# Optimization experiments

Measured on AMD Instinct MI355X. Metric: run time of the kernel, lower is better.

Reference implementation:

```python
import jax, jax.numpy as jnp
import numpy as np

N = 50000
E = 1600000
IN_CH = 128
HID = 16
HEADS = 8
OUT_CH = 1
NEG_SLOPE = 0.2


def setup_inputs() -> dict:
    key = jax.random.key(0)
    ks = jax.random.split(key, 12)
    x = jax.random.normal(ks[0], (N, IN_CH), dtype=jnp.float32)
    edge_index = jax.random.randint(ks[1], (2, E), 0, N, dtype=jnp.int64)
    s1 = 1.0 / np.sqrt(IN_CH)
    s2 = 1.0 / np.sqrt(HEADS * HID)
    W1 = jax.random.normal(ks[2], (IN_CH, HEADS * HID), dtype=jnp.float32) * s1
    att_src1 = jax.random.normal(ks[3], (HEADS, HID), dtype=jnp.float32) * s1
    att_dst1 = jax.random.normal(ks[4], (HEADS, HID), dtype=jnp.float32) * s1
    b1 = jnp.zeros((HEADS * HID,), dtype=jnp.float32)
    W2 = jax.random.normal(ks[5], (HEADS * HID, OUT_CH), dtype=jnp.float32) * s2
    att_src2 = jax.random.normal(ks[6], (1, OUT_CH), dtype=jnp.float32) * s2
    att_dst2 = jax.random.normal(ks[7], (1, OUT_CH), dtype=jnp.float32) * s2
    b2 = jnp.zeros((OUT_CH,), dtype=jnp.float32)
    return {"x": x, "edge_index": edge_index,
            "W1": W1, "att_src1": att_src1, "att_dst1": att_dst1, "b1": b1,
            "W2": W2, "att_src2": att_src2, "att_dst2": att_dst2, "b2": b2}


def gat_conv(x, src, dst, W, att_src, att_dst, b, heads, concat):
    n = x.shape[0]
    h = (x @ W).reshape(n, heads, -1)               # [N, H, C]
    a_s = jnp.einsum('nhc,hc->nh', h, att_src)      # [N, H]
    a_d = jnp.einsum('nhc,hc->nh', h, att_dst)
    e = jax.nn.leaky_relu(a_s[src] + a_d[dst], NEG_SLOPE)  # [E, H]
    # segment softmax over incoming edges of each dst node
    emax = jax.ops.segment_max(e, dst, num_segments=n)
    p = jnp.exp(e - emax[dst])
    denom = jax.ops.segment_sum(p, dst, num_segments=n)
    alpha = p / (denom[dst] + 1e-16)                 # [E, H]
    msg = h[src] * alpha[:, :, None]                 # [E, H, C]
    out = jax.ops.segment_sum(msg, dst, num_segments=n)  # [N, H, C]
    if concat:
        out = out.reshape(n, -1)
    else:
        out = out.mean(axis=1)
    return out + b


def reference(x, edge_index, W1, att_src1, att_dst1, b1, W2, att_src2, att_dst2, b2):
    n = x.shape[0]
    loops = jnp.arange(n, dtype=edge_index.dtype)
    src = jnp.concatenate([edge_index[0], loops])    # PyG add_self_loops=True
    dst = jnp.concatenate([edge_index[1], loops])
    h = gat_conv(x, src, dst, W1, att_src1, att_dst1, b1, HEADS, True)
    h = jax.nn.elu(h)
    out = gat_conv(h, src, dst, W2, att_src2, att_dst2, b2, 1, False)
    return out
```

## Files before the change

### kernel.cpp

```cpp
#include <hip/hip_runtime.h>
#include <hip/hip_fp16.h>
#include <math.h>

#define N_NODES 50000
#define N_EDGES 1600000
#define NEG 0.2f

#define PB 256
#define CHUNK ((N_EDGES + PB - 1) / PB)
#define BSHIFT 6
#define NBUCK ((N_NODES + 63) >> BSHIFT)


__global__ __launch_bounds__(1024) void count_pass(const int* __restrict__ ei, int* __restrict__ counts) {
    __shared__ int h[NBUCK];
    for (int i = threadIdx.x; i < NBUCK; i += 1024) h[i] = 0;
    __syncthreads();
    int p = blockIdx.x;
    int e0 = p * CHUNK, e1 = min(e0 + CHUNK, N_EDGES);
    for (int e = e0 + threadIdx.x; e < e1; e += 1024) {
        int d = ei[N_EDGES + e];
        atomicAdd(&h[d >> BSHIFT], 1);
    }
    __syncthreads();
    for (int i = threadIdx.x; i < NBUCK; i += 1024) counts[p * NBUCK + i] = h[i];
}

__global__ __launch_bounds__(256) void scan_blocks(const int* __restrict__ counts,
                                                   int* __restrict__ starts, int* __restrict__ btot) {
    __shared__ int s[256];
    int b = blockIdx.x;
    int v = counts[threadIdx.x * NBUCK + b];
    s[threadIdx.x] = v;
    __syncthreads();
    for (int off = 1; off < 256; off <<= 1) {
        int t = (threadIdx.x >= off) ? s[threadIdx.x - off] : 0;
        __syncthreads();
        s[threadIdx.x] += t;
        __syncthreads();
    }
    starts[threadIdx.x * NBUCK + b] = s[threadIdx.x] - v;
    if (threadIdx.x == 255) btot[b] = s[255];
}

__global__ __launch_bounds__(1024) void scan_total(const int* __restrict__ btot, int* __restrict__ bbase) {
    __shared__ int s[1024];
    int t = threadIdx.x;
    int v = (t < NBUCK) ? btot[t] : 0;
    s[t] = v;
    __syncthreads();
    for (int off = 1; off < 1024; off <<= 1) {
        int x = (t >= off) ? s[t - off] : 0;
        __syncthreads();
        s[t] += x;
        __syncthreads();
    }
    if (t < NBUCK) bbase[t] = s[t] - v;
    if (t == 0) bbase[NBUCK] = N_EDGES;
}

__global__ __launch_bounds__(1024) void bin_scatter(const int* __restrict__ ei, const int* __restrict__ starts,
                                                    const int* __restrict__ bbase, int* __restrict__ temp) {
    __shared__ int cur[NBUCK];
    int p = blockIdx.x;
    for (int i = threadIdx.x; i < NBUCK; i += 1024)
        cur[i] = bbase[i] + starts[p * NBUCK + i];
    __syncthreads();
    int e0 = p * CHUNK, e1 = min(e0 + CHUNK, N_EDGES);
    for (int e = e0 + threadIdx.x; e < e1; e += 1024) {
        int s = ei[e];
        int d = ei[N_EDGES + e];
        int b = d >> BSHIFT;
        int pos = atomicAdd(&cur[b], 1);
        temp[pos] = s | ((d & 63) << 16);
    }
}

__global__ __launch_bounds__(256) void csr_build(const int* __restrict__ temp, const int* __restrict__ bbase,
                                                 int* __restrict__ rowptr, int* __restrict__ csr_src) {
    __shared__ int cnt[64];
    __shared__ int cur[64];
    int b = blockIdx.x;
    int base = bbase[b];
    int nE = bbase[b + 1] - base;
    if (threadIdx.x < 64) cnt[threadIdx.x] = 0;
    __syncthreads();
    for (int i = threadIdx.x; i < nE; i += 256)
        atomicAdd(&cnt[temp[base + i] >> 16], 1);
    __syncthreads();
    if (threadIdx.x < 64) {
        int v = cnt[threadIdx.x];
        int incl = v;
#pragma unroll
        for (int off = 1; off < 64; off <<= 1) {
            int u = __shfl_up(incl, off, 64);
            if (threadIdx.x >= off) incl += u;
        }
        int excl = incl - v;
        cur[threadIdx.x] = base + excl;
        int node = (b << BSHIFT) + threadIdx.x;
        if (node <= N_NODES) rowptr[node] = base + excl;
    }
    __syncthreads();
    for (int i = threadIdx.x; i < nE; i += 256) {
        int v = temp[base + i];
        int pos = atomicAdd(&cur[v >> 16], 1);
        csr_src[pos] = v & 0xFFFF;
    }
}


__global__ __launch_bounds__(256) void gemm1_kernel(const float* __restrict__ x, const float* __restrict__ W1,
                                                    const float* __restrict__ att_s, const float* __restrict__ att_d,
                                                    __half2* __restrict__ h1, float* __restrict__ as1,
                                                    float* __restrict__ ad1) {
    __shared__ float xs[128][36];
    int n0 = blockIdx.x * 32;
    int t = threadIdx.x;
#pragma unroll
    for (int i = 0; i < 16; ++i) {
        int f = i * 256 + t;
        int r = f >> 7, c = f & 127;
        int gr = n0 + r;
        float v = (gr < N_NODES) ? x[(size_t)gr * 128 + c] : 0.f;
        xs[c][r] = v;
    }
    __syncthreads();
    int c0 = (t & 31) * 4;
    int r0 = (t >> 5) * 4;
    float acc[4][4];
#pragma unroll
    for (int i = 0; i < 4; ++i)
#pragma unroll
        for (int j = 0; j < 4; ++j) acc[i][j] = 0.f;
#pragma unroll 4
    for (int k = 0; k < 128; ++k) {
        float4 w = *(const float4*)(W1 + k * 128 + c0);
        float4 xr = *(const float4*)(&xs[k][r0]);
        float xv[4] = {xr.x, xr.y, xr.z, xr.w};
        float wv[4] = {w.x, w.y, w.z, w.w};
#pragma unroll
        for (int i = 0; i < 4; ++i)
#pragma unroll
            for (int j = 0; j < 4; ++j) acc[i][j] += xv[i] * wv[j];
    }
#pragma unroll
    for (int i = 0; i < 4; ++i) {
        int row = n0 + r0 + i;
        if (row < N_NODES) {
            __half2 p0 = __float22half2_rn(make_float2(acc[i][0], acc[i][1]));
            __half2 p1 = __float22half2_rn(make_float2(acc[i][2], acc[i][3]));
            h1[(size_t)row * 64 + (c0 >> 1)] = p0;
            h1[(size_t)row * 64 + (c0 >> 1) + 1] = p1;
        }
    }
    int head = (t & 31) >> 2;
    float ps[4], pd[4];
#pragma unroll
    for (int i = 0; i < 4; ++i) {
        float s = 0.f, d = 0.f;
#pragma unroll
        for (int j = 0; j < 4; ++j) {
            s += acc[i][j] * att_s[c0 + j];
            d += acc[i][j] * att_d[c0 + j];
        }
        ps[i] = s; pd[i] = d;
    }
#pragma unroll
    for (int i = 0; i < 4; ++i) {
        ps[i] += __shfl_xor(ps[i], 1, 64);
        ps[i] += __shfl_xor(ps[i], 2, 64);
        pd[i] += __shfl_xor(pd[i], 1, 64);
        pd[i] += __shfl_xor(pd[i], 2, 64);
    }
    if ((t & 3) == 0) {
#pragma unroll
        for (int i = 0; i < 4; ++i) {
            int row = n0 + r0 + i;
            if (row < N_NODES) {
                as1[row * 8 + head] = ps[i];
                ad1[row * 8 + head] = pd[i];
            }
        }
    }
}


__device__ __forceinline__ float lrelu(float v) { return fmaxf(v, NEG * v); }

__global__ __launch_bounds__(256) void agg1_kernel(const char* __restrict__ h1c, const char* __restrict__ as1c,
                                                   const float* __restrict__ ad1, const int* __restrict__ rowptr,
                                                   const int* __restrict__ csr_src, const float* __restrict__ b1,
                                                   const float* __restrict__ W2, float* __restrict__ h2out) {
    int lane = threadIdx.x & 63;
    int n = blockIdx.x * 4 + (threadIdx.x >> 6);
    if (n >= N_NODES) return;
    int hB = lane >> 3;
    int hP = lane & 7;
    unsigned lane4 = (unsigned)lane << 2;
    unsigned hP4 = (unsigned)hP << 2;
    int bperm_base = hB << 2;

    float adP = ad1[n * 8 + hP];
    float adC = ad1[n * 8 + hB];
    float asC = *(const float*)(as1c + ((unsigned)n * 32u + ((unsigned)hB << 2)));
    float p_self = __expf(lrelu(asC + adC));
    __half2 hvs = *(const __half2*)(h1c + (((unsigned)n << 8) + lane4));
    float acc0 = p_self * __half2float(__low2half(hvs));
    float acc1 = p_self * __half2float(__high2half(hvs));
    float l = p_self;

    int jb = rowptr[n], je = rowptr[n + 1];
    int deg = je - jb;
    int nchunks = deg >> 3;
    int j = jb;
    if (nchunks > 0) {
        int sP = csr_src[j + (lane >> 3)];
        float aP = *(const float*)(as1c + (((unsigned)sP << 5) + hP4));
        for (int c = 0; c < nchunks; ++c) {
            float pP = __expf(lrelu(aP + adP));
            int pPi = __float_as_int(pP);
            int sPc = sP;
            if (c + 1 < nchunks) {
                sP = csr_src[j + 8 + (lane >> 3)];
                aP = *(const float*)(as1c + (((unsigned)sP << 5) + hP4));
            }
#pragma unroll
            for (int e = 0; e < 8; ++e) {
                int addr = bperm_base + e * 32;
                float p = __int_as_float(__builtin_amdgcn_ds_bpermute(addr, pPi));
                int s = __builtin_amdgcn_ds_bpermute(addr, sPc);
                __half2 hv = *(const __half2*)(h1c + (((unsigned)s << 8) + lane4));
                acc0 += p * __half2float(__low2half(hv));
                acc1 += p * __half2float(__high2half(hv));
                l += p;
            }
            j += 8;
        }
    }
    if (j < je) {
        int r = je - j;
        int myj = j + (lane >> 3);
        int sP = 0;
        float pP = 0.f;
        if (myj < je) {
            sP = csr_src[myj];
            float aP = *(const float*)(as1c + (((unsigned)sP << 5) + hP4));
            pP = __expf(lrelu(aP + adP));
        }
        int pPi = __float_as_int(pP);
        for (int e = 0; e < r; ++e) {
            int addr = bperm_base + e * 32;
            float p = __int_as_float(__builtin_amdgcn_ds_bpermute(addr, pPi));
            int s = __builtin_amdgcn_ds_bpermute(addr, sP);
            __half2 hv = *(const __half2*)(h1c + (((unsigned)s << 8) + lane4));
            acc0 += p * __half2float(__low2half(hv));
            acc1 += p * __half2float(__high2half(hv));
            l += p;
        }
    }

    float inv = 1.f / (l + 1e-16f);
    int c0 = lane * 2;
    float y0 = acc0 * inv + b1[c0];
    float y1 = acc1 * inv + b1[c0 + 1];
    y0 = y0 > 0.f ? y0 : expm1f(y0);
    y1 = y1 > 0.f ? y1 : expm1f(y1);
    float part = y0 * W2[c0] + y1 * W2[c0 + 1];
    for (int off = 32; off; off >>= 1) part += __shfl_down(part, off, 64);
    if (lane == 0) h2out[n] = part;
}


__global__ __launch_bounds__(256) void agg2_kernel(const float* __restrict__ h2, const int* __restrict__ rowptr,
                                                   const int* __restrict__ csr_src, const float* __restrict__ att_s2,
                                                   const float* __restrict__ att_d2, const float* __restrict__ b2,
                                                   float* __restrict__ out) {
    int sub = threadIdx.x & 31;
    int n = blockIdx.x * 8 + (threadIdx.x >> 5);
    if (n >= N_NODES) return;
    float asw = att_s2[0], adw = att_d2[0];
    float h2n = h2[n];
    float ad = h2n * adw;
    float acc = 0.f, l = 0.f;
    if (sub == 0) {
        float p = __expf(lrelu(h2n * asw + ad));
        acc = p * h2n;
        l = p;
    }
    int jb = rowptr[n], je = rowptr[n + 1];
    for (int j = jb + sub; j < je; j += 32) {
        int s = csr_src[j];
        float hs = h2[s];
        float p = __expf(lrelu(hs * asw + ad));
        acc += p * hs;
        l += p;
    }
#pragma unroll
    for (int off = 16; off; off >>= 1) {
        acc += __shfl_down(acc, off, 32);
        l += __shfl_down(l, off, 32);
    }
    if (sub == 0) out[n] = acc / (l + 1e-16f) + b2[0];
}


extern "C" void kernel_launch(void* const* d_in, const int* in_sizes, int n_in,
                              void* d_out, int out_size, void* d_ws, size_t ws_size,
                              hipStream_t stream) {
    const float* x = (const float*)d_in[0];
    const int* ei = (const int*)d_in[1];
    const float* W1 = (const float*)d_in[2];
    const float* att_s1 = (const float*)d_in[3];
    const float* att_d1 = (const float*)d_in[4];
    const float* b1 = (const float*)d_in[5];
    const float* W2 = (const float*)d_in[6];
    const float* att_s2 = (const float*)d_in[7];
    const float* att_d2 = (const float*)d_in[8];
    const float* b2 = (const float*)d_in[9];
    float* out = (float*)d_out;

    char* p = (char*)d_ws;
    auto alloc = [&](size_t bytes) {
        char* q = p;
        p += (bytes + 255) & ~(size_t)255;
        return q;
    };
    int* counts = (int*)alloc((size_t)PB * NBUCK * 4);
    int* starts = (int*)alloc((size_t)PB * NBUCK * 4);
    int* btot = (int*)alloc((size_t)NBUCK * 4);
    int* bbase = (int*)alloc((size_t)(NBUCK + 1) * 4);
    int* rowptr = (int*)alloc((size_t)(N_NODES + 1) * 4);
    int* csr_src = (int*)alloc((size_t)N_EDGES * 4);
    __half2* h1 = (__half2*)alloc((size_t)N_NODES * 128 * 2);
    int* temp = (int*)h1;
    float* as1 = (float*)alloc((size_t)N_NODES * 8 * 4);
    float* ad1 = (float*)alloc((size_t)N_NODES * 8 * 4);
    float* h2 = (float*)alloc((size_t)N_NODES * 4);

    count_pass<<<PB, 1024, 0, stream>>>(ei, counts);
    scan_blocks<<<NBUCK, 256, 0, stream>>>(counts, starts, btot);
    scan_total<<<1, 1024, 0, stream>>>(btot, bbase);
    bin_scatter<<<PB, 1024, 0, stream>>>(ei, starts, bbase, temp);
    csr_build<<<NBUCK, 256, 0, stream>>>(temp, bbase, rowptr, csr_src);
    gemm1_kernel<<<(N_NODES + 31) / 32, 256, 0, stream>>>(x, W1, att_s1, att_d1, h1, as1, ad1);
    agg1_kernel<<<(N_NODES + 3) / 4, 256, 0, stream>>>((const char*)h1, (const char*)as1, ad1, rowptr,
                                                       csr_src, b1, W2, h2);
    agg2_kernel<<<(N_NODES + 7) / 8, 256, 0, stream>>>(h2, rowptr, csr_src, att_s2, att_d2, b2, out);
}
```

Measured before the change: 232.7 us.

## Locally sort edge chunks in LDS before coalesced bucket scatter

The binning scatter kernel now sorts each chunk of edges by destination bucket in shared memory, using a local histogram and scan. Each wave then writes whole bucket runs to global memory contiguously, replacing the scattered per-edge global stores. The partition count is halved to 128 so each chunk of 12500 ints (about 50KB) fits in LDS alongside the counters. The cost is fewer, heavier blocks with 256 threads and high LDS use, which limits occupancy, plus a duplicated count pass inside the scatter kernel.

```diff
diff --git a/kernel.cpp b/kernel.cpp
--- a/kernel.cpp
+++ b/kernel.cpp
@@ -6,8 +6,8 @@
 #define N_EDGES 1600000
 #define NEG 0.2f
 
-#define PB 256
-#define CHUNK ((N_EDGES + PB - 1) / PB)
+#define PB 128
+#define CHUNK (N_EDGES / PB)
 #define BSHIFT 6
 #define NBUCK ((N_NODES + 63) >> BSHIFT)
 
@@ -17,8 +17,8 @@
     for (int i = threadIdx.x; i < NBUCK; i += 1024) h[i] = 0;
     __syncthreads();
     int p = blockIdx.x;
-    int e0 = p * CHUNK, e1 = min(e0 + CHUNK, N_EDGES);
-    for (int e = e0 + threadIdx.x; e < e1; e += 1024) {
+    int e0 = p * CHUNK;
+    for (int e = e0 + threadIdx.x; e < e0 + CHUNK; e += 1024) {
         int d = ei[N_EDGES + e];
         atomicAdd(&h[d >> BSHIFT], 1);
     }
@@ -30,17 +30,18 @@
                                                    int* __restrict__ starts, int* __restrict__ btot) {
     __shared__ int s[256];
     int b = blockIdx.x;
-    int v = counts[threadIdx.x * NBUCK + b];
-    s[threadIdx.x] = v;
+    int t = threadIdx.x;
+    int v = (t < PB) ? counts[t * NBUCK + b] : 0;
+    s[t] = v;
     __syncthreads();
     for (int off = 1; off < 256; off <<= 1) {
-        int t = (threadIdx.x >= off) ? s[threadIdx.x - off] : 0;
-        __syncthreads();
-        s[threadIdx.x] += t;
-        __syncthreads();
-    }
-    starts[threadIdx.x * NBUCK + b] = s[threadIdx.x] - v;
-    if (threadIdx.x == 255) btot[b] = s[255];
+        int u = (t >= off) ? s[t - off] : 0;
+        __syncthreads();
+        s[t] += u;
+        __syncthreads();
+    }
+    if (t < PB) starts[t * NBUCK + b] = s[t] - v;
+    if (t == 255) btot[b] = s[255];
 }
 
 __global__ __launch_bounds__(1024) void scan_total(const int* __restrict__ btot, int* __restrict__ bbase) {
@@ -59,20 +60,62 @@
     if (t == 0) bbase[NBUCK] = N_EDGES;
 }
 
-__global__ __launch_bounds__(1024) void bin_scatter(const int* __restrict__ ei, const int* __restrict__ starts,
+__global__ __launch_bounds__(256) void sort_scatter(const int* __restrict__ ei, const int* __restrict__ starts,
                                                     const int* __restrict__ bbase, int* __restrict__ temp) {
+    __shared__ int cnt[NBUCK];
+    __shared__ int loff[NBUCK];
     __shared__ int cur[NBUCK];
-    int p = blockIdx.x;
-    for (int i = threadIdx.x; i < NBUCK; i += 1024)
-        cur[i] = bbase[i] + starts[p * NBUCK + i];
-    __syncthreads();
-    int e0 = p * CHUNK, e1 = min(e0 + CHUNK, N_EDGES);
-    for (int e = e0 + threadIdx.x; e < e1; e += 1024) {
+    __shared__ int sbuf[256];
+    __shared__ int ldata[CHUNK];
+    int p = blockIdx.x, t = threadIdx.x;
+    for (int i = t; i < NBUCK; i += 256) cnt[i] = 0;
+    __syncthreads();
+    int e0 = p * CHUNK;
+    for (int e = e0 + t; e < e0 + CHUNK; e += 256) {
+        int d = ei[N_EDGES + e];
+        atomicAdd(&cnt[d >> BSHIFT], 1);
+    }
+    __syncthreads();
+    int base = t * 4;
+    int c[4];
+    int sum = 0;
+#pragma unroll
+    for (int k = 0; k < 4; ++k) {
+        int b = base + k;
+        c[k] = (b < NBUCK) ? cnt[b] : 0;
+        sum += c[k];
+    }
+    sbuf[t] = sum;
+    __syncthreads();
+    for (int off = 1; off < 256; off <<= 1) {
+        int u = (t >= off) ? sbuf[t - off] : 0;
+        __syncthreads();
+        sbuf[t] += u;
+        __syncthreads();
+    }
+    int run = sbuf[t] - sum;
+#pragma unroll
+    for (int k = 0; k < 4; ++k) {
+        int b = base + k;
+        if (b < NBUCK) {
+            loff[b] = run;
+            cur[b] = run;
+            run += c[k];
+        }
+    }
+    __syncthreads();
+    for (int e = e0 + t; e < e0 + CHUNK; e += 256) {
         int s = ei[e];
         int d = ei[N_EDGES + e];
-        int b = d >> BSHIFT;
-        int pos = atomicAdd(&cur[b], 1);
-        temp[pos] = s | ((d & 63) << 16);
+        int pos = atomicAdd(&cur[d >> BSHIFT], 1);
+        ldata[pos] = s | ((d & 63) << 16);
+    }
+    __syncthreads();
+    int wv = t >> 6, ln = t & 63;
+    for (int b = wv; b < NBUCK; b += 4) {
+        int l0 = loff[b], len = cnt[b];
+        int g0 = bbase[b] + starts[p * NBUCK + b];
+        for (int k = ln; k < len; k += 64) temp[g0 + k] = ldata[l0 + k];
     }
 }
 
@@ -341,7 +384,7 @@
     count_pass<<<PB, 1024, 0, stream>>>(ei, counts);
     scan_blocks<<<NBUCK, 256, 0, stream>>>(counts, starts, btot);
     scan_total<<<1, 1024, 0, stream>>>(btot, bbase);
-    bin_scatter<<<PB, 1024, 0, stream>>>(ei, starts, bbase, temp);
+    sort_scatter<<<PB, 256, 0, stream>>>(ei, starts, bbase, temp);
     csr_build<<<NBUCK, 256, 0, stream>>>(temp, bbase, rowptr, csr_src);
     gemm1_kernel<<<(N_NODES + 31) / 32, 256, 0, stream>>>(x, W1, att_s1, att_d1, h1, as1, ad1);
     agg1_kernel<<<(N_NODES + 3) / 4, 256, 0, stream>>>((const char*)h1, (const char*)as1, ad1, rowptr,
```

Result: slower. 288.9 us (+24.1%).

## Fuse per-bucket CSR build into aggregation kernels using LDS-local edge lists

Applied to the files above, without the earlier changes.

Removes the separate csr_build kernel and its global rowptr/csr_src arrays. Each aggregation block now takes one 64-node bucket of binned edges, counts and sorts them into shared memory, and then aggregates those nodes from the LDS edge list. This saves a kernel launch and a global write and re-read of the CSR arrays, but the bucket sort is redone in both agg1 and agg2. The fixed LDSE=2816 buffer assumes no bucket holds more edges than that, which holds for uniform random graphs but could overflow otherwise. Parallelism drops to 782 blocks, each wave handling 8 nodes in sequence, and the old prefetch of the next chunk's sources is gone.

```diff
diff --git a/kernel.cpp b/kernel.cpp
--- a/kernel.cpp
+++ b/kernel.cpp
@@ -10,6 +10,7 @@
 #define CHUNK ((N_EDGES + PB - 1) / PB)
 #define BSHIFT 6
 #define NBUCK ((N_NODES + 63) >> BSHIFT)
+#define LDSE 2816
 
 
 __global__ __launch_bounds__(1024) void count_pass(const int* __restrict__ ei, int* __restrict__ counts) {
@@ -30,17 +31,18 @@
                                                    int* __restrict__ starts, int* __restrict__ btot) {
     __shared__ int s[256];
     int b = blockIdx.x;
-    int v = counts[threadIdx.x * NBUCK + b];
-    s[threadIdx.x] = v;
+    int t = threadIdx.x;
+    int v = counts[t * NBUCK + b];
+    s[t] = v;
     __syncthreads();
     for (int off = 1; off < 256; off <<= 1) {
-        int t = (threadIdx.x >= off) ? s[threadIdx.x - off] : 0;
+        int u = (t >= off) ? s[t - off] : 0;
         __syncthreads();
-        s[threadIdx.x] += t;
+        s[t] += u;
         __syncthreads();
     }
-    starts[threadIdx.x * NBUCK + b] = s[threadIdx.x] - v;
-    if (threadIdx.x == 255) btot[b] = s[255];
+    starts[t * NBUCK + b] = s[t] - v;
+    if (t == 255) btot[b] = s[255];
 }
 
 __global__ __launch_bounds__(1024) void scan_total(const int* __restrict__ btot, int* __restrict__ bbase) {
@@ -76,39 +78,6 @@
     }
 }
 
-__global__ __launch_bounds__(256) void csr_build(const int* __restrict__ temp, const int* __restrict__ bbase,
-                                                 int* __restrict__ rowptr, int* __restrict__ csr_src) {
-    __shared__ int cnt[64];
-    __shared__ int cur[64];
-    int b = blockIdx.x;
-    int base = bbase[b];
-    int nE = bbase[b + 1] - base;
-    if (threadIdx.x < 64) cnt[threadIdx.x] = 0;
-    __syncthreads();
-    for (int i = threadIdx.x; i < nE; i += 256)
-        atomicAdd(&cnt[temp[base + i] >> 16], 1);
-    __syncthreads();
-    if (threadIdx.x < 64) {
-        int v = cnt[threadIdx.x];
-        int incl = v;
-#pragma unroll
-        for (int off = 1; off < 64; off <<= 1) {
-            int u = __shfl_up(incl, off, 64);
-            if (threadIdx.x >= off) incl += u;
-        }
-        int excl = incl - v;
-        cur[threadIdx.x] = base + excl;
-        int node = (b << BSHIFT) + threadIdx.x;
-        if (node <= N_NODES) rowptr[node] = base + excl;
-    }
-    __syncthreads();
-    for (int i = threadIdx.x; i < nE; i += 256) {
-        int v = temp[base + i];
-        int pos = atomicAdd(&cur[v >> 16], 1);
-        csr_src[pos] = v & 0xFFFF;
-    }
-}
-
 
 __global__ __launch_bounds__(256) void gemm1_kernel(const float* __restrict__ x, const float* __restrict__ W1,
                                                     const float* __restrict__ att_s, const float* __restrict__ att_d,
@@ -188,120 +157,189 @@
 
 __device__ __forceinline__ float lrelu(float v) { return fmaxf(v, NEG * v); }
 
-__global__ __launch_bounds__(256) void agg1_kernel(const char* __restrict__ h1c, const char* __restrict__ as1c,
-                                                   const float* __restrict__ ad1, const int* __restrict__ rowptr,
-                                                   const int* __restrict__ csr_src, const float* __restrict__ b1,
+__global__ __launch_bounds__(512) void agg1_kernel(const char* __restrict__ h1c, const char* __restrict__ as1c,
+                                                   const float* __restrict__ ad1, const int* __restrict__ temp,
+                                                   const int* __restrict__ bbase, const float* __restrict__ b1,
                                                    const float* __restrict__ W2, float* __restrict__ h2out) {
-    int lane = threadIdx.x & 63;
-    int n = blockIdx.x * 4 + (threadIdx.x >> 6);
-    if (n >= N_NODES) return;
+    __shared__ int lsrc[LDSE];
+    __shared__ int cnt[64];
+    __shared__ int cur[64];
+    __shared__ int lrp[64];
+    int b = blockIdx.x, t = threadIdx.x;
+    int base = bbase[b];
+    int nE = bbase[b + 1] - base;
+    if (t < 64) cnt[t] = 0;
+    __syncthreads();
+    for (int i = t; i < nE; i += 512)
+        atomicAdd(&cnt[(unsigned)temp[base + i] >> 16], 1);
+    __syncthreads();
+    if (t < 64) {
+        int v = cnt[t];
+        int incl = v;
+#pragma unroll
+        for (int off = 1; off < 64; off <<= 1) {
+            int u = __shfl_up(incl, off, 64);
+            if (t >= off) incl += u;
+        }
+        int excl = incl - v;
+        lrp[t] = excl;
+        cur[t] = excl;
+    }
+    __syncthreads();
+    for (int i = t; i < nE; i += 512) {
+        int v = temp[base + i];
+        int pos = atomicAdd(&cur[(unsigned)v >> 16], 1);
+        lsrc[pos] = v & 0xFFFF;
+    }
+    __syncthreads();
+
+    int lane = t & 63;
+    int wave = t >> 6;
     int hB = lane >> 3;
     int hP = lane & 7;
     unsigned lane4 = (unsigned)lane << 2;
     unsigned hP4 = (unsigned)hP << 2;
     int bperm_base = hB << 2;
-
-    float adP = ad1[n * 8 + hP];
-    float adC = ad1[n * 8 + hB];
-    float asC = *(const float*)(as1c + ((unsigned)n * 32u + ((unsigned)hB << 2)));
-    float p_self = __expf(lrelu(asC + adC));
-    __half2 hvs = *(const __half2*)(h1c + (((unsigned)n << 8) + lane4));
-    float acc0 = p_self * __half2float(__low2half(hvs));
-    float acc1 = p_self * __half2float(__high2half(hvs));
-    float l = p_self;
-
-    int jb = rowptr[n], je = rowptr[n + 1];
-    int deg = je - jb;
-    int nchunks = deg >> 3;
-    int j = jb;
-    if (nchunks > 0) {
-        int sP = csr_src[j + (lane >> 3)];
-        float aP = *(const float*)(as1c + (((unsigned)sP << 5) + hP4));
-        for (int c = 0; c < nchunks; ++c) {
+    int prod = lane >> 3;
+
+    for (int kk = 0; kk < 8; ++kk) {
+        int k = wave * 8 + kk;
+        int n = b * 64 + k;
+        if (n >= N_NODES) continue;
+
+        float adP = ad1[n * 8 + hP];
+        float adC = ad1[n * 8 + hB];
+        float asC = *(const float*)(as1c + ((unsigned)n * 32u + ((unsigned)hB << 2)));
+        float p_self = __expf(lrelu(asC + adC));
+        __half2 hvs = *(const __half2*)(h1c + (((unsigned)n << 8) + lane4));
+        float acc0 = p_self * __half2float(__low2half(hvs));
+        float acc1 = p_self * __half2float(__high2half(hvs));
+        float l = p_self;
+
+        int jb = lrp[k];
+        int deg = cnt[k];
+        int j = 0;
+        for (; j + 8 <= deg; j += 8) {
+            int sP = lsrc[jb + j + prod];
+            float aP = *(const float*)(as1c + (((unsigned)sP << 5) + hP4));
             float pP = __expf(lrelu(aP + adP));
             int pPi = __float_as_int(pP);
-            int sPc = sP;
-            if (c + 1 < nchunks) {
-                sP = csr_src[j + 8 + (lane >> 3)];
-                aP = *(const float*)(as1c + (((unsigned)sP << 5) + hP4));
-            }
 #pragma unroll
             for (int e = 0; e < 8; ++e) {
                 int addr = bperm_base + e * 32;
                 float p = __int_as_float(__builtin_amdgcn_ds_bpermute(addr, pPi));
-                int s = __builtin_amdgcn_ds_bpermute(addr, sPc);
+                int s = __builtin_amdgcn_ds_bpermute(addr, sP);
                 __half2 hv = *(const __half2*)(h1c + (((unsigned)s << 8) + lane4));
                 acc0 += p * __half2float(__low2half(hv));
                 acc1 += p * __half2float(__high2half(hv));
                 l += p;
             }
-            j += 8;
-        }
-    }
-    if (j < je) {
-        int r = je - j;
-        int myj = j + (lane >> 3);
-        int sP = 0;
-        float pP = 0.f;
-        if (myj < je) {
-            sP = csr_src[myj];
-            float aP = *(const float*)(as1c + (((unsigned)sP << 5) + hP4));
-            pP = __expf(lrelu(aP + adP));
-        }
-        int pPi = __float_as_int(pP);
-        for (int e = 0; e < r; ++e) {
-            int addr = bperm_base + e * 32;
-            float p = __int_as_float(__builtin_amdgcn_ds_bpermute(addr, pPi));
-            int s = __builtin_amdgcn_ds_bpermute(addr, sP);
-            __half2 hv = *(const __half2*)(h1c + (((unsigned)s << 8) + lane4));
-            acc0 += p * __half2float(__low2half(hv));
-            acc1 += p * __half2float(__high2half(hv));
-            l += p;
-        }
-    }
-
-    float inv = 1.f / (l + 1e-16f);
-    int c0 = lane * 2;
-    float y0 = acc0 * inv + b1[c0];
-    float y1 = acc1 * inv + b1[c0 + 1];
-    y0 = y0 > 0.f ? y0 : expm1f(y0);
-    y1 = y1 > 0.f ? y1 : expm1f(y1);
-    float part = y0 * W2[c0] + y1 * W2[c0 + 1];
-    for (int off = 32; off; off >>= 1) part += __shfl_down(part, off, 64);
-    if (lane == 0) h2out[n] = part;
-}
-
-
-__global__ __launch_bounds__(256) void agg2_kernel(const float* __restrict__ h2, const int* __restrict__ rowptr,
-                                                   const int* __restrict__ csr_src, const float* __restrict__ att_s2,
+        }
+        if (j < deg) {
+            int r = deg - j;
+            int sP = 0;
+            float pP = 0.f;
+            if (j + prod < deg) {
+                sP = lsrc[jb + j + prod];
+                float aP = *(const float*)(as1c + (((unsigned)sP << 5) + hP4));
+                pP = __expf(lrelu(aP + adP));
+            }
+            int pPi = __float_as_int(pP);
+            for (int e = 0; e < r; ++e) {
+                int addr = bperm_base + e * 32;
+                float p = __int_as_float(__builtin_amdgcn_ds_bpermute(addr, pPi));
+                int s = __builtin_amdgcn_ds_bpermute(addr, sP);
+                __half2 hv = *(const __half2*)(h1c + (((unsigned)s << 8) + lane4));
+                acc0 += p * __half2float(__low2half(hv));
+                acc1 += p * __half2float(__high2half(hv));
+                l += p;
+            }
+        }
+
+        float inv = 1.f / (l + 1e-16f);
+        int c0 = lane * 2;
+        float y0 = acc0 * inv + b1[c0];
+        float y1 = acc1 * inv + b1[c0 + 1];
+        y0 = y0 > 0.f ? y0 : expm1f(y0);
+        y1 = y1 > 0.f ? y1 : expm1f(y1);
+        float part = y0 * W2[c0] + y1 * W2[c0 + 1];
+#pragma unroll
+        for (int off = 32; off; off >>= 1) part += __shfl_down(part, off, 64);
+        if (lane == 0) h2out[n] = part;
+    }
+}
+
+
+__global__ __launch_bounds__(256) void agg2_kernel(const float* __restrict__ h2, const int* __restrict__ temp,
+                                                   const int* __restrict__ bbase, const float* __restrict__ att_s2,
                                                    const float* __restrict__ att_d2, const float* __restrict__ b2,
                                                    float* __restrict__ out) {
-    int sub = threadIdx.x & 31;
-    int n = blockIdx.x * 8 + (threadIdx.x >> 5);
-    if (n >= N_NODES) return;
+    __shared__ int lsrc[LDSE];
+    __shared__ int cnt[64];
+    __shared__ int cur[64];
+    __shared__ int lrp[64];
+    int b = blockIdx.x, t = threadIdx.x;
+    int base = bbase[b];
+    int nE = bbase[b + 1] - base;
+    if (t < 64) cnt[t] = 0;
+    __syncthreads();
+    for (int i = t; i < nE; i += 256)
+        atomicAdd(&cnt[(unsigned)temp[base + i] >> 16], 1);
+    __syncthreads();
+    if (t < 64) {
+        int v = cnt[t];
+        int incl = v;
+#pragma unroll
+        for (int off = 1; off < 64; off <<= 1) {
+            int u = __shfl_up(incl, off, 64);
+            if (t >= off) incl += u;
+        }
+        int excl = incl - v;
+        lrp[t] = excl;
+        cur[t] = excl;
+    }
+    __syncthreads();
+    for (int i = t; i < nE; i += 256) {
+        int v = temp[base + i];
+        int pos = atomicAdd(&cur[(unsigned)v >> 16], 1);
+        lsrc[pos] = v & 0xFFFF;
+    }
+    __syncthreads();
+
     float asw = att_s2[0], adw = att_d2[0];
-    float h2n = h2[n];
-    float ad = h2n * adw;
-    float acc = 0.f, l = 0.f;
-    if (sub == 0) {
-        float p = __expf(lrelu(h2n * asw + ad));
-        acc = p * h2n;
-        l = p;
-    }
-    int jb = rowptr[n], je = rowptr[n + 1];
-    for (int j = jb + sub; j < je; j += 32) {
-        int s = csr_src[j];
-        float hs = h2[s];
-        float p = __expf(lrelu(hs * asw + ad));
-        acc += p * hs;
-        l += p;
-    }
-#pragma unroll
-    for (int off = 16; off; off >>= 1) {
-        acc += __shfl_down(acc, off, 32);
-        l += __shfl_down(l, off, 32);
-    }
-    if (sub == 0) out[n] = acc / (l + 1e-16f) + b2[0];
+    int lane = t & 63;
+    int wave = t >> 6;
+    int sub = lane & 7;
+    int grp = lane >> 3;
+    for (int round = 0; round < 2; ++round) {
+        int k = wave * 16 + round * 8 + grp;
+        int n = b * 64 + k;
+        float acc = 0.f, l = 0.f;
+        if (n < N_NODES) {
+            float h2n = h2[n];
+            float ad = h2n * adw;
+            if (sub == 0) {
+                float p = __expf(lrelu(h2n * asw + ad));
+                acc = p * h2n;
+                l = p;
+            }
+            int jb = lrp[k];
+            int deg = cnt[k];
+            for (int jj = sub; jj < deg; jj += 8) {
+                int s = lsrc[jb + jj];
+                float hs = h2[s];
+                float p = __expf(lrelu(hs * asw + ad));
+                acc += p * hs;
+                l += p;
+            }
+#pragma unroll
+            for (int off = 4; off; off >>= 1) {
+                acc += __shfl_down(acc, off, 8);
+                l += __shfl_down(l, off, 8);
+            }
+            if (sub == 0) out[n] = acc / (l + 1e-16f) + b2[0];
+        }
+    }
 }
 
 
@@ -330,10 +368,8 @@
     int* starts = (int*)alloc((size_t)PB * NBUCK * 4);
     int* btot = (int*)alloc((size_t)NBUCK * 4);
     int* bbase = (int*)alloc((size_t)(NBUCK + 1) * 4);
-    int* rowptr = (int*)alloc((size_t)(N_NODES + 1) * 4);
-    int* csr_src = (int*)alloc((size_t)N_EDGES * 4);
+    int* temp = (int*)alloc((size_t)N_EDGES * 4);
     __half2* h1 = (__half2*)alloc((size_t)N_NODES * 128 * 2);
-    int* temp = (int*)h1;
     float* as1 = (float*)alloc((size_t)N_NODES * 8 * 4);
     float* ad1 = (float*)alloc((size_t)N_NODES * 8 * 4);
     float* h2 = (float*)alloc((size_t)N_NODES * 4);
@@ -342,9 +378,7 @@
     scan_blocks<<<NBUCK, 256, 0, stream>>>(counts, starts, btot);
     scan_total<<<1, 1024, 0, stream>>>(btot, bbase);
     bin_scatter<<<PB, 1024, 0, stream>>>(ei, starts, bbase, temp);
-    csr_build<<<NBUCK, 256, 0, stream>>>(temp, bbase, rowptr, csr_src);
     gemm1_kernel<<<(N_NODES + 31) / 32, 256, 0, stream>>>(x, W1, att_s1, att_d1, h1, as1, ad1);
-    agg1_kernel<<<(N_NODES + 3) / 4, 256, 0, stream>>>((const char*)h1, (const char*)as1, ad1, rowptr,
-                                                       csr_src, b1, W2, h2);
-    agg2_kernel<<<(N_NODES + 7) / 8, 256, 0, stream>>>(h2, rowptr, csr_src, att_s2, att_d2, b2, out);
-}
+    agg1_kernel<<<NBUCK, 512, 0, stream>>>((const char*)h1, (const char*)as1, ad1, temp, bbase, b1, W2, h2);
+    agg2_kernel<<<NBUCK, 256, 0, stream>>>(h2, temp, bbase, att_s2, att_d2, b2, out);
+}
```

After: 234.6 us. Within noise of the previous version (+0.8%).
